# Optimization experiments

Hardware: AMD Instinct MI355X
Metric: run time of the kernel (lower is better)

The kernel has to match this reference:

```python
import jax, jax.numpy as jnp
import numpy as np
from jax import lax

B, K = 16, 10
C_IN, C_OUT = 32, 64
H_IN, W_IN = 32, 32
KS, STRIDE, PAD = 3, 1, 1
H_OUT = (H_IN + 2 * PAD - KS) // STRIDE + 1
W_OUT = (W_IN + 2 * PAD - KS) // STRIDE + 1


def setup_inputs() -> dict:
    key = jax.random.key(0)
    k1, k2, k3 = jax.random.split(key, 3)
    x = jax.random.normal(k1, (B, K, C_IN, H_IN, W_IN), dtype=jnp.float32)
    # init_local (non-mono, non-first): std = 1/sqrt(0.5 * in_ch * k^2)
    std = 1.0 / np.sqrt(0.5 * C_IN * KS ** 2)
    weight = jax.random.normal(k2, (H_OUT, W_OUT, C_OUT, C_IN, KS, KS), dtype=jnp.float32) * std
    bias = jax.random.normal(k3, (K, C_OUT, H_OUT, W_OUT), dtype=jnp.float32) * 0.01
    return {"x": x, "weight": weight, "bias": bias}


def reference(x, weight, bias):
    # x: [B, K, C_in, H, W] -> merge batch and category dims
    b, k = x.shape[:2]
    xr = x.reshape((b * k,) + x.shape[2:])  # [BK, C_in, H, W]
    # Extract all kxk patches in one fused op: [BK, C_in*KS*KS, h_out, w_out]
    # feature dim ordered (c, kh, kw) -- matches weight layout [o, i, kh, kw].
    patches = lax.conv_general_dilated_patches(
        xr, filter_shape=(KS, KS), window_strides=(STRIDE, STRIDE),
        padding=[(PAD, PAD), (PAD, PAD)])
    w2 = weight.reshape(H_OUT, W_OUT, C_OUT, C_IN * KS * KS)  # [i, j, o, f]
    # Per-pixel unshared contraction (block-diagonal batched GEMM)
    out = jnp.einsum('bfij,ijof->boij', patches, w2)  # [BK, C_out, h_out, w_out]
    out = out.reshape(b, k, C_OUT, H_OUT, W_OUT)
    return out + bias[None]
```

## Files before the change

### kernel.cpp

```cpp
#include <hip/hip_runtime.h>


#define HW    32
#define CIN   32
#define COUT  64
#define FDIM  288
#define FPAD  296
#define NBK   160
#define HP    34
#define PLANE (NBK * CIN)
#define SLOT_SH (3 * PLANE)
#define WOFF  (4 * SLOT_SH)

using f32x4  = __attribute__((ext_vector_type(4))) float;
using bf16x8 = __attribute__((ext_vector_type(8))) short;
using s16x4  = __attribute__((ext_vector_type(4))) short;

static __device__ inline unsigned short f2bf(float f) {
    unsigned u = __float_as_uint(f);
    u += 0x7FFFu + ((u >> 16) & 1u);
    return (unsigned short)(u >> 16);
}
static __device__ inline void gl_lds16(const short* src, short* dst) {
    __builtin_amdgcn_global_load_lds(
        (const __attribute__((address_space(1))) unsigned int*)src,
        (__attribute__((address_space(3))) unsigned int*)dst, 16, 0, 0);
}
static constexpr size_t XC_BYTES = (size_t)HP * HP * PLANE * 2;
static constexpr size_t CO_BYTES = (size_t)1024 * COUT * NBK * 2;

__global__ __launch_bounds__(256) void hz_kernel(short* __restrict__ xc)
{
    const int id = blockIdx.x;
    int h, w;
    if (id < 34)      { h = 0;  w = id; }
    else if (id < 68) { h = 33; w = id - 34; }
    else { const int e = id - 68; h = 1 + (e >> 1); w = (e & 1) * 33; }
    uint2* p = reinterpret_cast<uint2*>(xc + (size_t)(h * HP + w) * PLANE);
    const uint2 z = {0u, 0u};
#pragma unroll
    for (int r = 0; r < 5; ++r)
        p[threadIdx.x + r * 256] = z;
}

__global__ __launch_bounds__(256) void t1_kernel(
    const float* __restrict__ x, short* __restrict__ xc)
{
    __shared__ short tile[HW][36];
    const int bid = blockIdx.x;
    const int bk  = bid >> 5;
    const int h   = bid & 31;
    const int tid = threadIdx.x;
    {
        const int c  = tid >> 3;
        const int w4 = (tid & 7) * 4;
        const float4 v = *reinterpret_cast<const float4*>(
            x + (size_t)(bk * 32 + c) * 1024 + h * 32 + w4);
        tile[w4 + 0][c] = (short)f2bf(v.x);
        tile[w4 + 1][c] = (short)f2bf(v.y);
        tile[w4 + 2][c] = (short)f2bf(v.z);
        tile[w4 + 3][c] = (short)f2bf(v.w);
    }
    __syncthreads();
    {
        const int w  = tid >> 3;
        const int cq = tid & 7;
        const uint2 pk = *reinterpret_cast<const uint2*>(&tile[w][cq * 4]);
        const int sidx = bk * 32 + ((cq * 4) ^ (((bk >> 1) & 3) << 3));
        *reinterpret_cast<uint2*>(
            xc + (size_t)((h + 1) * HP + (w + 1)) * PLANE + sidx) = pk;
    }
}

#define SB()  __builtin_amdgcn_sched_barrier(0)
#define VM(n) { asm volatile("s_waitcnt vmcnt(" #n ")" ::: "memory"); SB(); }
#define LG0BAR() { asm volatile("s_waitcnt lgkmcnt(0)" ::: "memory"); SB(); \
                   __builtin_amdgcn_s_barrier(); SB(); }
#define BARA() { asm volatile("s_waitcnt lgkmcnt(0)" ::: "memory"); SB(); \
                 __builtin_amdgcn_s_barrier(); SB(); }

__global__ __launch_bounds__(512) void local2d_p_kernel(
    const short* __restrict__ xc,
    const float* __restrict__ w,
    short* __restrict__ co)
{
    __shared__ __align__(1024) short Sl[WOFF + COUT * FPAD];

    const int hb = blockIdx.x;
    const int lb = (hb & 7) * 32 + (hb >> 3);
    const int i  = lb >> 3;
    const int jt = lb & 7;
    const int j0 = jt * 4;
    const int tid = threadIdx.x;

    const int wave = tid >> 6;
    const int lane = tid & 63;
    const int nt   = wave & 3;
    const int mh   = wave >> 2;
    const int l15  = lane & 15;
    const int lg   = lane >> 4;
    const int lg8  = lg * 8;

    short* WL = Sl + WOFF;

    int rowbyte[5];
#pragma unroll
    for (int mt = 0; mt < 5; ++mt) {
        const int bk = mh * 80 + mt * 16 + l15;
        rowbyte[mt] = (bk * 64 + lg * 16) ^ (((bk >> 1) & 3) << 4);
    }

    float4 wv0[9], wv1[9];
    const f32x4 z4 = {0.f, 0.f, 0.f, 0.f};
    f32x4 acc0, acc1, acc2, acc3, acc4;

#define WISSUE(dst, pp) {                                                  \
        const float* wp = w + (size_t)((i * 32) + j0 + (pp)) * (COUT * FDIM); \
        _Pragma("unroll")                                                  \
        for (int q = 0; q < 9; ++q) {                                      \
            const int g  = tid + q * 512;                                  \
            const int o2 = g / 72;                                         \
            const int f4 = (g - o2 * 72) * 4;                              \
            dst[q] = *reinterpret_cast<const float4*>(wp + o2 * FDIM + f4);\
        } SB(); }

#define SCATTER(src) {                                                     \
        _Pragma("unroll")                                                  \
        for (int q = 0; q < 9; ++q) {                                      \
            const int g  = tid + q * 512;                                  \
            const int o2 = g / 72;                                         \
            const int f4 = (g - o2 * 72) * 4;                              \
            const float vv[4] = {src[q].x, src[q].y, src[q].z, src[q].w};  \
            short* wrow = WL + o2 * FPAD;                                  \
            _Pragma("unroll")                                              \
            for (int e = 0; e < 4; ++e) {                                  \
                const int f = f4 + e; const int c = f / 9;                 \
                const int cell = f - c * 9;                                \
                wrow[cell * 32 + c] = (short)f2bf(vv[e]); } } SB(); }

#define RISSUE(s) {                                                        \
        if (tid < 480) {                                                   \
            _Pragma("unroll")                                              \
            for (int r = 0; r < 4; ++r) {                                  \
                const int u  = tid + r * 480;                              \
                const int pl = u / 640;                                    \
                const int cu = u - pl * 640;                               \
                const short* src = xc + (size_t)((i + pl) * HP + (j0 + 4 + (s))) * PLANE + cu * 8; \
                gl_lds16(src, Sl + (size_t)((s) * SLOT_SH) + (size_t)u * 8); \
            } } SB(); }

#define COMPUTE(p) {                                                       \
        acc0 = z4; acc1 = z4; acc2 = z4; acc3 = z4; acc4 = z4;             \
        const short* bp = WL + (nt * 16 + l15) * FPAD + lg8;               \
        _Pragma("unroll")                                                  \
        for (int kc = 0; kc < 9; ++kc) {                                   \
            const int kh   = kc / 3;                                       \
            const int kw   = kc - kh * 3;                                  \
            const int slot = ((p) + kw) & 3;                               \
            const char* ab = (const char*)Sl + slot * (SLOT_SH * 2) + kh * (PLANE * 2); \
            const bf16x8 b  = *reinterpret_cast<const bf16x8*>(bp + kc * 32); \
            const bf16x8 a0 = *reinterpret_cast<const bf16x8*>(ab + rowbyte[0]); \
            const bf16x8 a1 = *reinterpret_cast<const bf16x8*>(ab + rowbyte[1]); \
            const bf16x8 a2 = *reinterpret_cast<const bf16x8*>(ab + rowbyte[2]); \
            const bf16x8 a3 = *reinterpret_cast<const bf16x8*>(ab + rowbyte[3]); \
            const bf16x8 a4 = *reinterpret_cast<const bf16x8*>(ab + rowbyte[4]); \
            acc0 = __builtin_amdgcn_mfma_f32_16x16x32_bf16(a0, b, acc0, 0, 0, 0); \
            acc1 = __builtin_amdgcn_mfma_f32_16x16x32_bf16(a1, b, acc1, 0, 0, 0); \
            acc2 = __builtin_amdgcn_mfma_f32_16x16x32_bf16(a2, b, acc2, 0, 0, 0); \
            acc3 = __builtin_amdgcn_mfma_f32_16x16x32_bf16(a3, b, acc3, 0, 0, 0); \
            acc4 = __builtin_amdgcn_mfma_f32_16x16x32_bf16(a4, b, acc4, 0, 0, 0); \
        } }

#define STORE(p) {                                                         \
        const int pix = i * 32 + j0 + (p);                                 \
        const int o3  = nt * 16 + l15;                                     \
        const size_t cb = ((size_t)pix * COUT + o3) * NBK + mh * 80 + lg * 4; \
        { s16x4 s_; s_.x = (short)f2bf(acc0[0]); s_.y = (short)f2bf(acc0[1]); \
          s_.z = (short)f2bf(acc0[2]); s_.w = (short)f2bf(acc0[3]);        \
          *reinterpret_cast<s16x4*>(co + cb + 0) = s_; }                   \
        { s16x4 s_; s_.x = (short)f2bf(acc1[0]); s_.y = (short)f2bf(acc1[1]); \
          s_.z = (short)f2bf(acc1[2]); s_.w = (short)f2bf(acc1[3]);        \
          *reinterpret_cast<s16x4*>(co + cb + 16) = s_; }                  \
        { s16x4 s_; s_.x = (short)f2bf(acc2[0]); s_.y = (short)f2bf(acc2[1]); \
          s_.z = (short)f2bf(acc2[2]); s_.w = (short)f2bf(acc2[3]);        \
          *reinterpret_cast<s16x4*>(co + cb + 32) = s_; }                  \
        { s16x4 s_; s_.x = (short)f2bf(acc3[0]); s_.y = (short)f2bf(acc3[1]); \
          s_.z = (short)f2bf(acc3[2]); s_.w = (short)f2bf(acc3[3]);        \
          *reinterpret_cast<s16x4*>(co + cb + 48) = s_; }                  \
        { s16x4 s_; s_.x = (short)f2bf(acc4[0]); s_.y = (short)f2bf(acc4[1]); \
          s_.z = (short)f2bf(acc4[2]); s_.w = (short)f2bf(acc4[3]);        \
          *reinterpret_cast<s16x4*>(co + cb + 64) = s_; } }

    WISSUE(wv0, 0)
    {
#pragma unroll
        for (int r = 0; r < 15; ++r) {
            const int u   = tid + r * 512;
            const int s   = u / 1920;
            const int rem = u - s * 1920;
            const int pl  = rem / 640;
            const int cu  = rem - pl * 640;
            const short* src = xc + (size_t)((i + pl) * HP + (j0 + s)) * PLANE + cu * 8;
            gl_lds16(src, Sl + (size_t)u * 8);
        }
        SB();
    }
    VM(15)
    SCATTER(wv0)
    WISSUE(wv1, 1)
    VM(9)
    LG0BAR()

    COMPUTE(0) STORE(0)
    BARA()
    VM(0)
    SCATTER(wv1)
    WISSUE(wv0, 2)
    LG0BAR()

    RISSUE(0)
    COMPUTE(1) STORE(1)
    BARA()
    VM(4)
    SCATTER(wv0)
    WISSUE(wv1, 3)
    VM(9)
    LG0BAR()

    RISSUE(1)
    COMPUTE(2) STORE(2)
    BARA()
    VM(4)
    SCATTER(wv1)
    VM(0)
    LG0BAR()

    COMPUTE(3) STORE(3)

#undef WISSUE
#undef SCATTER
#undef RISSUE
#undef COMPUTE
#undef STORE
}

__global__ __launch_bounds__(256) void t2_kernel(
    const short* __restrict__ co,
    const float* __restrict__ bias,
    float* __restrict__ out)
{
    __shared__ short tl[32][36];
    const int b    = blockIdx.x;
    const int o    = b & 63;
    const int rest = b >> 6;
    const int bkT  = rest % 5;
    const int pixT = rest / 5;
    const int tid  = threadIdx.x;
    {
        const int p  = tid >> 3;
        const int bq = tid & 7;
        const int pix = pixT * 32 + p;
        const s16x4 v = *reinterpret_cast<const s16x4*>(
            co + ((size_t)pix * COUT + o) * NBK + bkT * 32 + bq * 4);
        *reinterpret_cast<s16x4*>(&tl[p][bq * 4]) = v;
    }
    __syncthreads();
    {
        const int bb = tid >> 3;
        const int pq = tid & 7;
        const int bk = bkT * 32 + bb;
        const int k  = bk % 10;
        const size_t pbase = (size_t)pixT * 32 + pq * 4;
        const float4 bv = *reinterpret_cast<const float4*>(
            bias + ((size_t)(k * COUT + o) << 10) + pbase);
        float4 r;
        r.x = __uint_as_float(((unsigned)(unsigned short)tl[pq * 4 + 0][bb]) << 16) + bv.x;
        r.y = __uint_as_float(((unsigned)(unsigned short)tl[pq * 4 + 1][bb]) << 16) + bv.y;
        r.z = __uint_as_float(((unsigned)(unsigned short)tl[pq * 4 + 2][bb]) << 16) + bv.z;
        r.w = __uint_as_float(((unsigned)(unsigned short)tl[pq * 4 + 3][bb]) << 16) + bv.w;
        *reinterpret_cast<float4*>(out + ((size_t)(bk * COUT + o) << 10) + pbase) = r;
    }
}

__global__ __launch_bounds__(256) void xpose_kernel(
    const float* __restrict__ x, short* __restrict__ xc)
{
    __shared__ short tile[HW][36];
    const int bid = blockIdx.x;
    const int bk  = bid >> 5;
    const int h   = bid & 31;
    const int tid = threadIdx.x;
    {
        const int c  = tid >> 3;
        const int w4 = (tid & 7) * 4;
        const float4 v = *reinterpret_cast<const float4*>(
            x + (size_t)(bk * 32 + c) * 1024 + h * 32 + w4);
        tile[w4 + 0][c] = (short)f2bf(v.x);
        tile[w4 + 1][c] = (short)f2bf(v.y);
        tile[w4 + 2][c] = (short)f2bf(v.z);
        tile[w4 + 3][c] = (short)f2bf(v.w);
    }
    __syncthreads();
    {
        const int w  = tid >> 3;
        const int cq = tid & 7;
        const uint2 pk = *reinterpret_cast<const uint2*>(&tile[w][cq * 4]);
        *reinterpret_cast<uint2*>(
            xc + ((size_t)(bk * 1024 + h * 32 + w) * 32 + cq * 4)) = pk;
    }
}

__global__ __launch_bounds__(512, 4) void local2d_mfma2_kernel(
    const short* __restrict__ xc,
    const float* __restrict__ w,
    const float* __restrict__ bias,
    float* __restrict__ out)
{
    __shared__ short Wl[COUT * FPAD];
    const int hb  = blockIdx.x;
    const int lb  = (hb & 7) * 128 + (hb >> 3);
    const int i   = lb >> 5;
    const int j   = lb & 31;
    const int pix = i * HW + j;
    const int tid = threadIdx.x;
    {
        const float* wp = w + (size_t)pix * (COUT * FDIM);
#pragma unroll
        for (int p = 0; p < 9; ++p) {
            const int g  = tid + p * 512;
            const int o  = g / 72;
            const int f4 = (g - o * 72) * 4;
            const float4 v = *reinterpret_cast<const float4*>(wp + o * FDIM + f4);
            const float vv[4] = {v.x, v.y, v.z, v.w};
            short* wrow = &Wl[o * FPAD];
#pragma unroll
            for (int e = 0; e < 4; ++e) {
                const int f    = f4 + e;
                const int c    = f / 9;
                const int cell = f - c * 9;
                wrow[cell * 32 + c] = (short)f2bf(vv[e]);
            }
        }
    }
    __syncthreads();
    const int wave = tid >> 6;
    const int lane = tid & 63;
    const int nt   = wave & 3;
    const int mh   = wave >> 2;
    const int l15  = lane & 15;
    const int lg8  = (lane >> 4) * 8;
    f32x4 acc[5];
#pragma unroll
    for (int mt = 0; mt < 5; ++mt)
#pragma unroll
        for (int r = 0; r < 4; ++r) acc[mt][r] = 0.f;
    const short* xb[5];
#pragma unroll
    for (int mt = 0; mt < 5; ++mt) {
        const int bk = mh * 80 + mt * 16 + l15;
        xb[mt] = xc + (size_t)bk * (HW * HW * CIN) + lg8;
    }
    const short* bp = &Wl[(nt * 16 + l15) * FPAD + lg8];
#pragma unroll
    for (int kc = 0; kc < 9; ++kc) {
        const int kh = kc / 3;
        const int kw = kc - kh * 3;
        const int ih = i - 1 + kh;
        const int jw = j - 1 + kw;
        if ((unsigned)ih >= (unsigned)HW || (unsigned)jw >= (unsigned)HW)
            continue;
        const bf16x8 b = *reinterpret_cast<const bf16x8*>(bp + kc * 32);
        const int xoff = (ih * HW + jw) * CIN;
#pragma unroll
        for (int mt = 0; mt < 5; ++mt) {
            const bf16x8 a = *reinterpret_cast<const bf16x8*>(xb[mt] + xoff);
            acc[mt] = __builtin_amdgcn_mfma_f32_16x16x32_bf16(a, b, acc[mt], 0, 0, 0);
        }
    }
    const int o  = nt * 16 + l15;
    const int r0 = (lane >> 4) * 4;
#pragma unroll
    for (int mt = 0; mt < 5; ++mt) {
        const int bk0 = mh * 80 + mt * 16 + r0;
#pragma unroll
        for (int r = 0; r < 4; ++r) {
            const int bk = bk0 + r;
            const int k  = bk % 10;
            out[((size_t)(bk * COUT + o) << 10) + pix] =
                acc[mt][r] + bias[((size_t)(k * COUT + o) << 10) + pix];
        }
    }
}

extern "C" void kernel_launch(void* const* d_in, const int* in_sizes, int n_in,
                              void* d_out, int out_size, void* d_ws, size_t ws_size,
                              hipStream_t stream) {
    const float* x    = (const float*)d_in[0];
    const float* w    = (const float*)d_in[1];
    const float* bias = (const float*)d_in[2];
    float* out        = (float*)d_out;

    if (ws_size >= XC_BYTES + CO_BYTES) {
        short* xc = (short*)d_ws;
        short* co = (short*)((char*)d_ws + XC_BYTES);
        hipLaunchKernelGGL(hz_kernel, dim3(132), dim3(256), 0, stream, xc);
        hipLaunchKernelGGL(t1_kernel, dim3(5120), dim3(256), 0, stream, x, xc);
        hipLaunchKernelGGL(local2d_p_kernel, dim3(256), dim3(512), 0, stream,
                           xc, w, co);
        hipLaunchKernelGGL(t2_kernel, dim3(10240), dim3(256), 0, stream,
                           co, bias, out);
    } else {
        short* xc = (short*)d_ws;
        hipLaunchKernelGGL(xpose_kernel, dim3(5120), dim3(256), 0, stream, x, xc);
        hipLaunchKernelGGL(local2d_mfma2_kernel, dim3(1024), dim3(512), 0, stream,
                           xc, w, bias, out);
    }
}
```

Measured before the change: 51.09 us.

## Fuse bias epilogue into local conv kernel via LDS transpose, drop t2 pass

The main conv kernel now keeps all four pixels' accumulators in registers and, at the end, stages them as bf16 in LDS. It then writes the final NCHW fp32 output with bias added directly, instead of writing an intermediate bf16 buffer that a separate transpose/bias kernel re-read. This removes one kernel launch and a round trip of the intermediate tensor through global memory. It also adds s_setprio around the MFMA loops. The cost is 80 accumulator VGPRs held live across the whole pipeline, which may raise register pressure or cause spills, and the output stores are only 16-byte chunks per (bk,o) row.

```diff
diff --git a/kernel.cpp b/kernel.cpp
--- a/kernel.cpp
+++ b/kernel.cpp
@@ -11,6 +11,7 @@
 #define PLANE (NBK * CIN)
 #define SLOT_SH (3 * PLANE)
 #define WOFF  (4 * SLOT_SH)
+#define BKP   164
 
 using f32x4  = __attribute__((ext_vector_type(4))) float;
 using bf16x8 = __attribute__((ext_vector_type(8))) short;
@@ -21,13 +22,15 @@
     u += 0x7FFFu + ((u >> 16) & 1u);
     return (unsigned short)(u >> 16);
 }
+static __device__ inline float bf2f(short h) {
+    return __uint_as_float(((unsigned)(unsigned short)h) << 16);
+}
 static __device__ inline void gl_lds16(const short* src, short* dst) {
     __builtin_amdgcn_global_load_lds(
         (const __attribute__((address_space(1))) unsigned int*)src,
         (__attribute__((address_space(3))) unsigned int*)dst, 16, 0, 0);
 }
 static constexpr size_t XC_BYTES = (size_t)HP * HP * PLANE * 2;
-static constexpr size_t CO_BYTES = (size_t)1024 * COUT * NBK * 2;
 
 __global__ __launch_bounds__(256) void hz_kernel(short* __restrict__ xc)
 {
@@ -79,10 +82,11 @@
 #define BARA() { asm volatile("s_waitcnt lgkmcnt(0)" ::: "memory"); SB(); \
                  __builtin_amdgcn_s_barrier(); SB(); }
 
-__global__ __launch_bounds__(512) void local2d_p_kernel(
+__global__ __launch_bounds__(512) void local2d_e_kernel(
     const short* __restrict__ xc,
     const float* __restrict__ w,
-    short* __restrict__ co)
+    const float* __restrict__ bias,
+    float* __restrict__ out)
 {
     __shared__ __align__(1024) short Sl[WOFF + COUT * FPAD];
 
@@ -112,7 +116,11 @@
 
     float4 wv0[9], wv1[9];
     const f32x4 z4 = {0.f, 0.f, 0.f, 0.f};
-    f32x4 acc0, acc1, acc2, acc3, acc4;
+    f32x4 acc[4][5];
+#pragma unroll
+    for (int p = 0; p < 4; ++p)
+#pragma unroll
+        for (int mt = 0; mt < 5; ++mt) acc[p][mt] = z4;
 
 #define WISSUE(dst, pp) {                                                  \
         const float* wp = w + (size_t)((i * 32) + j0 + (pp)) * (COUT * FDIM); \
@@ -150,8 +158,8 @@
             } } SB(); }
 
 #define COMPUTE(p) {                                                       \
-        acc0 = z4; acc1 = z4; acc2 = z4; acc3 = z4; acc4 = z4;             \
         const short* bp = WL + (nt * 16 + l15) * FPAD + lg8;               \
+        __builtin_amdgcn_s_setprio(1);                                     \
         _Pragma("unroll")                                                  \
         for (int kc = 0; kc < 9; ++kc) {                                   \
             const int kh   = kc / 3;                                       \
@@ -164,32 +172,13 @@
             const bf16x8 a2 = *reinterpret_cast<const bf16x8*>(ab + rowbyte[2]); \
             const bf16x8 a3 = *reinterpret_cast<const bf16x8*>(ab + rowbyte[3]); \
             const bf16x8 a4 = *reinterpret_cast<const bf16x8*>(ab + rowbyte[4]); \
-            acc0 = __builtin_amdgcn_mfma_f32_16x16x32_bf16(a0, b, acc0, 0, 0, 0); \
-            acc1 = __builtin_amdgcn_mfma_f32_16x16x32_bf16(a1, b, acc1, 0, 0, 0); \
-            acc2 = __builtin_amdgcn_mfma_f32_16x16x32_bf16(a2, b, acc2, 0, 0, 0); \
-            acc3 = __builtin_amdgcn_mfma_f32_16x16x32_bf16(a3, b, acc3, 0, 0, 0); \
-            acc4 = __builtin_amdgcn_mfma_f32_16x16x32_bf16(a4, b, acc4, 0, 0, 0); \
-        } }
-
-#define STORE(p) {                                                         \
-        const int pix = i * 32 + j0 + (p);                                 \
-        const int o3  = nt * 16 + l15;                                     \
-        const size_t cb = ((size_t)pix * COUT + o3) * NBK + mh * 80 + lg * 4; \
-        { s16x4 s_; s_.x = (short)f2bf(acc0[0]); s_.y = (short)f2bf(acc0[1]); \
-          s_.z = (short)f2bf(acc0[2]); s_.w = (short)f2bf(acc0[3]);        \
-          *reinterpret_cast<s16x4*>(co + cb + 0) = s_; }                   \
-        { s16x4 s_; s_.x = (short)f2bf(acc1[0]); s_.y = (short)f2bf(acc1[1]); \
-          s_.z = (short)f2bf(acc1[2]); s_.w = (short)f2bf(acc1[3]);        \
-          *reinterpret_cast<s16x4*>(co + cb + 16) = s_; }                  \
-        { s16x4 s_; s_.x = (short)f2bf(acc2[0]); s_.y = (short)f2bf(acc2[1]); \
-          s_.z = (short)f2bf(acc2[2]); s_.w = (short)f2bf(acc2[3]);        \
-          *reinterpret_cast<s16x4*>(co + cb + 32) = s_; }                  \
-        { s16x4 s_; s_.x = (short)f2bf(acc3[0]); s_.y = (short)f2bf(acc3[1]); \
-          s_.z = (short)f2bf(acc3[2]); s_.w = (short)f2bf(acc3[3]);        \
-          *reinterpret_cast<s16x4*>(co + cb + 48) = s_; }                  \
-        { s16x4 s_; s_.x = (short)f2bf(acc4[0]); s_.y = (short)f2bf(acc4[1]); \
-          s_.z = (short)f2bf(acc4[2]); s_.w = (short)f2bf(acc4[3]);        \
-          *reinterpret_cast<s16x4*>(co + cb + 64) = s_; } }
+            acc[p][0] = __builtin_amdgcn_mfma_f32_16x16x32_bf16(a0, b, acc[p][0], 0, 0, 0); \
+            acc[p][1] = __builtin_amdgcn_mfma_f32_16x16x32_bf16(a1, b, acc[p][1], 0, 0, 0); \
+            acc[p][2] = __builtin_amdgcn_mfma_f32_16x16x32_bf16(a2, b, acc[p][2], 0, 0, 0); \
+            acc[p][3] = __builtin_amdgcn_mfma_f32_16x16x32_bf16(a3, b, acc[p][3], 0, 0, 0); \
+            acc[p][4] = __builtin_amdgcn_mfma_f32_16x16x32_bf16(a4, b, acc[p][4], 0, 0, 0); \
+        }                                                                  \
+        __builtin_amdgcn_s_setprio(0); }
 
     WISSUE(wv0, 0)
     {
@@ -211,7 +200,7 @@
     VM(9)
     LG0BAR()
 
-    COMPUTE(0) STORE(0)
+    COMPUTE(0)
     BARA()
     VM(0)
     SCATTER(wv1)
@@ -219,7 +208,7 @@
     LG0BAR()
 
     RISSUE(0)
-    COMPUTE(1) STORE(1)
+    COMPUTE(1)
     BARA()
     VM(4)
     SCATTER(wv0)
@@ -228,58 +217,57 @@
     LG0BAR()
 
     RISSUE(1)
-    COMPUTE(2) STORE(2)
+    COMPUTE(2)
     BARA()
     VM(4)
     SCATTER(wv1)
     VM(0)
     LG0BAR()
 
-    COMPUTE(3) STORE(3)
+    COMPUTE(3)
+    BARA()
+
+    {
+        short* col = Sl;
+        const int o3 = nt * 16 + l15;
+#pragma unroll
+        for (int p = 0; p < 4; ++p) {
+#pragma unroll
+            for (int mt = 0; mt < 5; ++mt) {
+                s16x4 s_;
+                s_.x = (short)f2bf(acc[p][mt][0]);
+                s_.y = (short)f2bf(acc[p][mt][1]);
+                s_.z = (short)f2bf(acc[p][mt][2]);
+                s_.w = (short)f2bf(acc[p][mt][3]);
+                *reinterpret_cast<s16x4*>(
+                    &col[(p * COUT + o3) * BKP + mh * 80 + mt * 16 + lg * 4]) = s_;
+            }
+        }
+        LG0BAR()
+
+        const int pix0 = i * 32 + j0;
+#pragma unroll
+        for (int s = 0; s < 20; ++s) {
+            const int id = tid + s * 512;
+            const int o  = id & 63;
+            const int bk = id >> 6;
+            const int k  = bk % 10;
+            const float4 bv = *reinterpret_cast<const float4*>(
+                bias + (((size_t)(k * COUT + o)) << 10) + pix0);
+            float4 r;
+            r.x = bf2f(col[(0 * COUT + o) * BKP + bk]) + bv.x;
+            r.y = bf2f(col[(1 * COUT + o) * BKP + bk]) + bv.y;
+            r.z = bf2f(col[(2 * COUT + o) * BKP + bk]) + bv.z;
+            r.w = bf2f(col[(3 * COUT + o) * BKP + bk]) + bv.w;
+            *reinterpret_cast<float4*>(
+                out + (((size_t)(bk * COUT + o)) << 10) + pix0) = r;
+        }
+    }
 
 #undef WISSUE
 #undef SCATTER
 #undef RISSUE
 #undef COMPUTE
-#undef STORE
-}
-
-__global__ __launch_bounds__(256) void t2_kernel(
-    const short* __restrict__ co,
-    const float* __restrict__ bias,
-    float* __restrict__ out)
-{
-    __shared__ short tl[32][36];
-    const int b    = blockIdx.x;
-    const int o    = b & 63;
-    const int rest = b >> 6;
-    const int bkT  = rest % 5;
-    const int pixT = rest / 5;
-    const int tid  = threadIdx.x;
-    {
-        const int p  = tid >> 3;
-        const int bq = tid & 7;
-        const int pix = pixT * 32 + p;
-        const s16x4 v = *reinterpret_cast<const s16x4*>(
-            co + ((size_t)pix * COUT + o) * NBK + bkT * 32 + bq * 4);
-        *reinterpret_cast<s16x4*>(&tl[p][bq * 4]) = v;
-    }
-    __syncthreads();
-    {
-        const int bb = tid >> 3;
-        const int pq = tid & 7;
-        const int bk = bkT * 32 + bb;
-        const int k  = bk % 10;
-        const size_t pbase = (size_t)pixT * 32 + pq * 4;
-        const float4 bv = *reinterpret_cast<const float4*>(
-            bias + ((size_t)(k * COUT + o) << 10) + pbase);
-        float4 r;
-        r.x = __uint_as_float(((unsigned)(unsigned short)tl[pq * 4 + 0][bb]) << 16) + bv.x;
-        r.y = __uint_as_float(((unsigned)(unsigned short)tl[pq * 4 + 1][bb]) << 16) + bv.y;
-        r.z = __uint_as_float(((unsigned)(unsigned short)tl[pq * 4 + 2][bb]) << 16) + bv.z;
-        r.w = __uint_as_float(((unsigned)(unsigned short)tl[pq * 4 + 3][bb]) << 16) + bv.w;
-        *reinterpret_cast<float4*>(out + ((size_t)(bk * COUT + o) << 10) + pbase) = r;
-    }
 }
 
 __global__ __launch_bounds__(256) void xpose_kernel(
@@ -400,15 +388,12 @@
     const float* bias = (const float*)d_in[2];
     float* out        = (float*)d_out;
 
-    if (ws_size >= XC_BYTES + CO_BYTES) {
+    if (ws_size >= XC_BYTES) {
         short* xc = (short*)d_ws;
-        short* co = (short*)((char*)d_ws + XC_BYTES);
         hipLaunchKernelGGL(hz_kernel, dim3(132), dim3(256), 0, stream, xc);
         hipLaunchKernelGGL(t1_kernel, dim3(5120), dim3(256), 0, stream, x, xc);
-        hipLaunchKernelGGL(local2d_p_kernel, dim3(256), dim3(512), 0, stream,
-                           xc, w, co);
-        hipLaunchKernelGGL(t2_kernel, dim3(10240), dim3(256), 0, stream,
-                           co, bias, out);
+        hipLaunchKernelGGL(local2d_e_kernel, dim3(256), dim3(512), 0, stream,
+                           xc, w, bias, out);
     } else {
         short* xc = (short*)d_ws;
         hipLaunchKernelGGL(xpose_kernel, dim3(5120), dim3(256), 0, stream, x, xc);
```

Measured after the change: 57.69 us. +12.9%, slower.
